# Kernel optimization log

Measured on AMD Instinct MI355X. Metric: run time of the kernel, lower is better.

The kernel has to match this reference:

```python
import jax, jax.numpy as jnp
import numpy as np

INIT_L = 512.0
EPS = 1e-6
N_HEAD = 16


def fire_bias(T, w1, b1, w2, b2, c, L_multiplier):
    # positions and relative distances
    pos = jnp.arange(T, dtype=jnp.float32)
    rel = pos[:, None] - pos[None, :]                      # (T, T)
    threshold = jnp.abs(L_multiplier * INIT_L)
    pos_norm = jnp.maximum(pos, threshold)[:, None]        # (T, 1)
    rel = jnp.log(jnp.abs(c * rel) + 1.0)                  # (T, T)
    pos_norm = jnp.log(jnp.abs(c * pos_norm) + 1.0) + EPS  # (T, 1)
    nd = rel / pos_norm                                    # (T, T)
    # tiny MLP: 1 -> mlp_width -> n_head
    h = jax.nn.relu(nd[..., None] * w1[0] + b1)            # (T, T, 32)
    bias = jnp.einsum('tsw,wh->hts', h, w2) + b2[:, None, None]  # (H, T, T)
    causal = jnp.tril(jnp.ones((T, T), dtype=bool))
    bias = jnp.where(causal[None], bias, -jnp.inf)
    return bias[None]                                      # (1, H, T, T)


def reference(x, Wqkv, bqkv, Wproj, bproj, w1, b1, w2, b2, c_param, L_multiplier):
    B, T, C = x.shape
    H = N_HEAD
    hd = C // H
    qkv = x @ Wqkv + bqkv                                  # (B, T, 3C)
    q, k, v = jnp.split(qkv, 3, axis=-1)
    q = q.reshape(B, T, H, hd).transpose(0, 2, 1, 3)       # (B, H, T, hd)
    k = k.reshape(B, T, H, hd).transpose(0, 2, 1, 3)
    v = v.reshape(B, T, H, hd).transpose(0, 2, 1, 3)
    bias = fire_bias(T, w1, b1, w2, b2, c_param, L_multiplier)  # (1, H, T, T)
    scale = 1.0 / jnp.sqrt(jnp.float32(hd))
    att = jnp.einsum('bhqd,bhkd->bhqk', q, k) * scale + bias
    att = jax.nn.softmax(att, axis=-1)
    y = jnp.einsum('bhqk,bhkd->bhqd', att, v)              # (B, H, T, hd)
    y = y.transpose(0, 2, 1, 3).reshape(B, T, C)
    return y @ Wproj + bproj


def setup_inputs() -> dict:
    key = jax.random.key(0)
    ks = jax.random.split(key, 8)
    B, T, C, H, W = 2, 2048, 1024, 16, 32
    s = 0.02
    return {
        'x': jax.random.normal(ks[0], (B, T, C), jnp.float32),
        'Wqkv': jax.random.normal(ks[1], (C, 3 * C), jnp.float32) * s,
        'bqkv': jnp.zeros((3 * C,), jnp.float32),
        'Wproj': jax.random.normal(ks[2], (C, C), jnp.float32) * s,
        'bproj': jnp.zeros((C,), jnp.float32),
        'w1': jax.random.normal(ks[3], (1, W), jnp.float32),
        'b1': jnp.zeros((W,), jnp.float32),
        'w2': jax.random.normal(ks[4], (W, H), jnp.float32) * 0.1,
        'b2': jnp.zeros((H,), jnp.float32),
        'c_param': jnp.float32(0.1),
        'L_multiplier': jnp.float32(1.0),
    }
```

## Files before the change

kernel.cpp:

```cpp
#include <hip/hip_runtime.h>
#include <cstdint>

typedef unsigned short u16;
typedef unsigned int u32;

typedef short bf16x8 __attribute__((ext_vector_type(8)));
typedef float f32x4 __attribute__((ext_vector_type(4)));

#define LN2 0.69314718055994530942f
#define LOG2E 1.44269504088896340736f
#define INFF __builtin_inff()

__device__ __forceinline__ u16 f2bf(float f) {
  u32 u = __float_as_uint(f);
  u = (u + 0x7fffu + ((u >> 16) & 1u)) >> 16;
  return (u16)u;
}
__device__ __forceinline__ u16 f2bfr(float f) {
  return (u16)((__float_as_uint(f) + 0x8000u) >> 16);
}
__device__ __forceinline__ u32 pack2bf(float a, float b) {
  u32 ta = __float_as_uint(a) + 0x8000u;
  u32 tb = __float_as_uint(b) + 0x8000u;
  return __builtin_amdgcn_perm(tb, ta, 0x07060302u);
}

#if __has_builtin(__builtin_amdgcn_global_load_lds)
#define HAVE_GLDS 1
__device__ __forceinline__ void glds16(const u16* g, u16* l) {
  __builtin_amdgcn_global_load_lds((const __attribute__((address_space(1))) void*)g,
                                   (__attribute__((address_space(3))) void*)l, 16, 0, 0);
}
#else
#define HAVE_GLDS 0
#endif


__global__ void k_convert_x(const float* __restrict__ in, u16* __restrict__ out, int n4) {
  int i = blockIdx.x * blockDim.x + threadIdx.x;
  if (i < n4) {
    float4 v = ((const float4*)in)[i];
    ushort4 o;
    o.x = f2bf(v.x); o.y = f2bf(v.y); o.z = f2bf(v.z); o.w = f2bf(v.w);
    ((ushort4*)out)[i] = o;
  }
}

__global__ void k_transpose_bf(const float* __restrict__ in, u16* __restrict__ out, int R, int C) {
  __shared__ float t[32][33];
  int c0 = blockIdx.x * 32, r0 = blockIdx.y * 32;
  int tx = threadIdx.x, ty = threadIdx.y;
#pragma unroll
  for (int k = 0; k < 4; k++) t[ty + 8 * k][tx] = in[(size_t)(r0 + ty + 8 * k) * C + c0 + tx];
  __syncthreads();
#pragma unroll
  for (int k = 0; k < 4; k++) out[(size_t)(c0 + ty + 8 * k) * R + r0 + tx] = f2bf(t[tx][ty + 8 * k]);
}

__global__ void k_tables(const float* __restrict__ cP, const float* __restrict__ lP,
                         float* __restrict__ ig2, float* __restrict__ rl) {
  int t = blockIdx.x * blockDim.x + threadIdx.x;
  float c = fabsf(cP[0]);
  if (t < 2048) {
    float lm = lP[0];
    float thr = fabsf(lm * 512.0f);
    float pn = fmaxf((float)t, thr);
    float den = logf(c * pn + 1.0f) + 1e-6f;
    ig2[t] = LN2 / den;
  }
  if (t < 2112) {
    int d = t - 63;
    if (d < 0) d = 0;
    rl[t] = log2f(c * (float)d + 1.0f);
  }
}

__global__ void k_segments(const float* __restrict__ w1, const float* __restrict__ b1,
                           const float* __restrict__ w2, const float* __restrict__ b2,
                           float* __restrict__ segX, float* __restrict__ segA,
                           float* __restrict__ segB, int* __restrict__ segU) {
  __shared__ float xs[32];
  __shared__ float srt[32];
  __shared__ float uniq[32];
  __shared__ int uCnt;
  int t = threadIdx.x;
  if (t < 32) {
    float w = w1[t], b = b1[t];
    xs[t] = (w != 0.0f) ? (-b / w) : INFF;
  }
  __syncthreads();
  if (t < 32) {
    float x = xs[t];
    int r = 0;
    for (int v = 0; v < 32; v++) {
      float xv = xs[v];
      if (xv < x || (xv == x && v < t)) r++;
    }
    srt[r] = x;
  }
  __syncthreads();
  if (t == 0) {
    int u = 0;
    for (int i = 0; i < 32; i++) {
      float v = srt[i];
      if (v < 3.0e38f && (u == 0 || v != uniq[u - 1])) uniq[u++] = v;
    }
    uCnt = u;
    segU[0] = u;
  }
  __syncthreads();
  int u = uCnt;
  if (t < u) segX[t] = uniq[t];
  for (int idx = t; idx < (u + 1) * 16; idx += blockDim.x) {
    int j = idx >> 4, h = idx & 15;
    float p;
    if (u == 0) p = 0.0f;
    else if (j == 0) p = uniq[0] - 1.0f;
    else if (j == u) p = uniq[u - 1] + 1.0f;
    else p = 0.5f * (uniq[j - 1] + uniq[j]);
    float A = b2[h], B = 0.0f;
    for (int w = 0; w < 32; w++) {
      float w1w = w1[w], b1w = b1[w], w2wh = w2[w * 16 + h];
      if (w1w != 0.0f) {
        if (fmaf(w1w, p, b1w) > 0.0f) { B += w1w * w2wh; A += b1w * w2wh; }
      } else if (b1w > 0.0f) {
        A += b1w * w2wh;
      }
    }
    segA[j * 16 + h] = A;
    segB[j * 16 + h] = B;
  }
}

template <int MODE>
__launch_bounds__(256, 3)
__global__ void k_gemm(const u16* __restrict__ A, const u16* __restrict__ BT,
                       const float* __restrict__ bias, float* __restrict__ outF,
                       u16* __restrict__ outQ, u16* __restrict__ outK, u16* __restrict__ outV,
                       int M, int N, int K) {
#if HAVE_GLDS
  __shared__ u16 As[128 * 64];
  __shared__ u16 Bs[128 * 64];
  const int tid = threadIdx.x;
  const int lane = tid & 63, wave = tid >> 6;
  const int li = lane & 15, quad = lane >> 4;
  const int wrow = (wave >> 1) * 64, wcol = (wave & 1) * 64;
  const int rb = blockIdx.y * 128, cb = blockIdx.x * 128;

  f32x4 acc[4][4];
#pragma unroll
  for (int i = 0; i < 4; i++)
#pragma unroll
    for (int j = 0; j < 4; j++) acc[i][j] = (f32x4){0.f, 0.f, 0.f, 0.f};

  const u16* gA = A + (size_t)(rb + (tid >> 3)) * K + (tid & 7) * 8;
  const u16* gB = BT + (size_t)(cb + (tid >> 3)) * K + (tid & 7) * 8;
  u16* lA = As + wave * 512;
  u16* lB = Bs + wave * 512;

  for (int k0 = 0; k0 < K; k0 += 64) {
    __syncthreads();
#pragma unroll
    for (int ch = 0; ch < 4; ch++) {
      glds16(gA + (size_t)ch * 32 * K + k0, lA + ch * 2048);
      glds16(gB + (size_t)ch * 32 * K + k0, lB + ch * 2048);
    }
    __syncthreads();
#pragma unroll
    for (int c = 0; c < 2; c++) {
      bf16x8 af[4], bfr[4];
#pragma unroll
      for (int mt = 0; mt < 4; mt++)
        af[mt] = *(const bf16x8*)(&As[(wrow + mt * 16 + li) * 64 + c * 32 + quad * 8]);
#pragma unroll
      for (int nt = 0; nt < 4; nt++)
        bfr[nt] = *(const bf16x8*)(&Bs[(wcol + nt * 16 + li) * 64 + c * 32 + quad * 8]);
#pragma unroll
      for (int mt = 0; mt < 4; mt++)
#pragma unroll
        for (int nt = 0; nt < 4; nt++)
          acc[mt][nt] = __builtin_amdgcn_mfma_f32_16x16x32_bf16(af[mt], bfr[nt], acc[mt][nt], 0, 0, 0);
    }
  }
#else
  __shared__ u16 As[128][72];
  __shared__ u16 Bs[128][72];
  const int tid = threadIdx.x;
  const int lane = tid & 63, wave = tid >> 6;
  const int li = lane & 15, quad = lane >> 4;
  const int wrow = (wave >> 1) * 64, wcol = (wave & 1) * 64;
  const int rb = blockIdx.y * 128, cb = blockIdx.x * 128;
  const int srow = tid >> 1, shalf = tid & 1;

  f32x4 acc[4][4];
#pragma unroll
  for (int i = 0; i < 4; i++)
#pragma unroll
    for (int j = 0; j < 4; j++) acc[i][j] = (f32x4){0.f, 0.f, 0.f, 0.f};

  const u16* gA = A + (size_t)(rb + srow) * K + shalf * 32;
  const u16* gB = BT + (size_t)(cb + srow) * K + shalf * 32;

  for (int k0 = 0; k0 < K; k0 += 64) {
    uint4 a0 = *(const uint4*)(gA + k0);
    uint4 a1 = *(const uint4*)(gA + k0 + 8);
    uint4 a2 = *(const uint4*)(gA + k0 + 16);
    uint4 a3 = *(const uint4*)(gA + k0 + 24);
    uint4 b0 = *(const uint4*)(gB + k0);
    uint4 b1 = *(const uint4*)(gB + k0 + 8);
    uint4 b2v = *(const uint4*)(gB + k0 + 16);
    uint4 b3 = *(const uint4*)(gB + k0 + 24);
    __syncthreads();
    *(uint4*)(&As[srow][shalf * 32]) = a0;
    *(uint4*)(&As[srow][shalf * 32 + 8]) = a1;
    *(uint4*)(&As[srow][shalf * 32 + 16]) = a2;
    *(uint4*)(&As[srow][shalf * 32 + 24]) = a3;
    *(uint4*)(&Bs[srow][shalf * 32]) = b0;
    *(uint4*)(&Bs[srow][shalf * 32 + 8]) = b1;
    *(uint4*)(&Bs[srow][shalf * 32 + 16]) = b2v;
    *(uint4*)(&Bs[srow][shalf * 32 + 24]) = b3;
    __syncthreads();
#pragma unroll
    for (int c = 0; c < 2; c++) {
      bf16x8 af[4], bfr[4];
#pragma unroll
      for (int mt = 0; mt < 4; mt++)
        af[mt] = *(const bf16x8*)(&As[wrow + mt * 16 + li][c * 32 + quad * 8]);
#pragma unroll
      for (int nt = 0; nt < 4; nt++)
        bfr[nt] = *(const bf16x8*)(&Bs[wcol + nt * 16 + li][c * 32 + quad * 8]);
#pragma unroll
      for (int mt = 0; mt < 4; mt++)
#pragma unroll
        for (int nt = 0; nt < 4; nt++)
          acc[mt][nt] = __builtin_amdgcn_mfma_f32_16x16x32_bf16(af[mt], bfr[nt], acc[mt][nt], 0, 0, 0);
    }
  }
#endif

#pragma unroll
  for (int mt = 0; mt < 4; mt++)
#pragma unroll
    for (int nt = 0; nt < 4; nt++)
#pragma unroll
      for (int r = 0; r < 4; r++) {
        int row = rb + wrow + mt * 16 + quad * 4 + r;
        int col = cb + wcol + nt * 16 + li;
        float v = acc[mt][nt][r] + bias[col];
        if (MODE == 0) {
          int b = row >> 11, tt = row & 2047;
          int sel = col >> 10, w = col & 1023, h = w >> 6, dd = w & 63;
          u16* dst = (sel == 0) ? outQ : ((sel == 1) ? outK : outV);
          dst[(size_t)((b * 16 + h) * 2048 + tt) * 64 + dd] = f2bf(v);
        } else {
          outF[(size_t)row * N + col] = v;
        }
      }
}

__launch_bounds__(256, 2)
__global__ void k_attn(const u16* __restrict__ Q, const u16* __restrict__ K,
                       const u16* __restrict__ V, u16* __restrict__ Y,
                       const float* __restrict__ ig2, const float* __restrict__ RL,
                       const float* __restrict__ segX, const float* __restrict__ segA,
                       const float* __restrict__ segB, const int* __restrict__ segU) {
  __shared__ u16 Ks[2][64][72];
  __shared__ u16 Vts[2][64][72];
  __shared__ u16 Ps[64][72];
  __shared__ float rls[2112];
  __shared__ float sXl[32];
  __shared__ float sAl[33];
  __shared__ float sBl[33];

  const int pr = blockIdx.x, h = blockIdx.y, b = blockIdx.z;
  const int tid = threadIdx.x, lane = tid & 63, wave = tid >> 6;
  const int li = lane & 15, quad = lane >> 4;
  const int bh = b * 16 + h;
  const u16* Qg = Q + (size_t)bh * 2048 * 64;
  const u16* Kg = K + (size_t)bh * 2048 * 64;
  const u16* Vg = V + (size_t)bh * 2048 * 64;

  for (int i = tid; i < 2112; i += 256) rls[i] = RL[i];

  const int u = segU[0];
  float x0 = INFF, A0, B0, A1, B1;
  A0 = segA[h]; B0 = segB[h]; A1 = A0; B1 = B0;
  if (u == 1) { x0 = segX[0]; A1 = segA[16 + h]; B1 = segB[16 + h]; }
  if (u > 1) {
    if (tid < u) sXl[tid] = segX[tid];
    if (tid < u + 1) { sAl[tid] = segA[tid * 16 + h]; sBl[tid] = segB[tid * 16 + h]; }
  }
  const float A0e = A0 * LOG2E, A1e = A1 * LOG2E;
  const float SCL = 0.125f * LOG2E;

  auto run_tile = [&](int qt) {
    const int qw = qt * 64 + wave * 16;
    const int t = qw + li;
    bf16x8 qf[2];
#pragma unroll
    for (int c = 0; c < 2; c++)
      qf[c] = *(const bf16x8*)(Qg + (size_t)t * 64 + c * 32 + quad * 8);

    const float gI = ig2[t];
    const float x0r = x0 / gI;
    const float B0g = B0 * gI * LOG2E, B1g = B1 * gI * LOG2E;
    float mrow = -INFF, lrow = 0.0f;
    f32x4 oacc[4];
#pragma unroll
    for (int nt = 0; nt < 4; nt++) oacc[nt] = (f32x4){0.f, 0.f, 0.f, 0.f};

    uint4 kv0, kv1, w0, w1;
    {
      const u16* ksrc = Kg + (size_t)(tid >> 2) * 64 + (tid & 3) * 16;
      kv0 = *(const uint4*)(ksrc);
      kv1 = *(const uint4*)(ksrc + 8);
      const u16* vsrc = Vg + (size_t)(2 * (tid & 31)) * 64 + (tid >> 5) * 8;
      w0 = *(const uint4*)(vsrc);
      w1 = *(const uint4*)(vsrc + 64);
    }
    __syncthreads();

    for (int kt = 0; kt <= qt; kt++) {
      const int kb = kt * 64, buf = kt & 1;
      *(uint4*)(&Ks[buf][tid >> 2][(tid & 3) * 16]) = kv0;
      *(uint4*)(&Ks[buf][tid >> 2][(tid & 3) * 16 + 8]) = kv1;
      {
        const int kkp = tid & 31, d0 = (tid >> 5) * 8;
        const u16* pw0 = (const u16*)&w0;
        const u16* pw1 = (const u16*)&w1;
#pragma unroll
        for (int j = 0; j < 8; j++)
          *(u32*)(&Vts[buf][d0 + j][2 * kkp]) = (u32)pw0[j] | ((u32)pw1[j] << 16);
      }
      __syncthreads();
      if (kt < qt) {
        const u16* ksrc = Kg + (size_t)(kb + 64 + (tid >> 2)) * 64 + (tid & 3) * 16;
        kv0 = *(const uint4*)(ksrc);
        kv1 = *(const uint4*)(ksrc + 8);
        const u16* vsrc = Vg + (size_t)(kb + 64 + 2 * (tid & 31)) * 64 + (tid >> 5) * 8;
        w0 = *(const uint4*)(vsrc);
        w1 = *(const uint4*)(vsrc + 64);
      }

      f32x4 sacc[4];
#pragma unroll
      for (int nt = 0; nt < 4; nt++) sacc[nt] = (f32x4){0.f, 0.f, 0.f, 0.f};
#pragma unroll
      for (int c = 0; c < 2; c++)
#pragma unroll
        for (int nt = 0; nt < 4; nt++) {
          bf16x8 kf = *(const bf16x8*)(&Ks[buf][nt * 16 + li][c * 32 + quad * 8]);
          sacc[nt] = __builtin_amdgcn_mfma_f32_16x16x32_bf16(kf, qf[c], sacc[nt], 0, 0, 0);
        }

      const int Cbase = t - kb - quad * 4 + 63;
      const float* rp = &rls[Cbase - 51];
      if (u <= 1) {
        const int lim = Cbase - 63;
#pragma unroll
        for (int nt = 0; nt < 4; nt++)
#pragma unroll
          for (int r = 0; r < 4; r++) {
            float rlv = rp[51 - nt * 16 - r];
            bool hi = rlv > x0r;
            float z = fmaf(rlv, hi ? B1g : B0g, hi ? A1e : A0e);
            z = fmaf(sacc[nt][r], SCL, z);
            if (kt == qt) z = (nt * 16 + r > lim) ? -INFF : z;
            sacc[nt][r] = z;
          }
      } else {
        const int lim = Cbase - 63;
#pragma unroll
        for (int nt = 0; nt < 4; nt++)
#pragma unroll
          for (int r = 0; r < 4; r++) {
            float nd = rp[51 - nt * 16 - r] * gI;
            int j = 0;
            for (int i = 0; i < u; i++) j += (nd > sXl[i]) ? 1 : 0;
            float z = (fmaf(nd, sBl[j], sAl[j]) + sacc[nt][r] * 0.125f) * LOG2E;
            if (kt == qt) z = (nt * 16 + r > lim) ? -INFF : z;
            sacc[nt][r] = z;
          }
      }

      float vm = -INFF;
#pragma unroll
      for (int nt = 0; nt < 4; nt++)
#pragma unroll
        for (int r = 0; r < 4; r++) vm = fmaxf(vm, sacc[nt][r]);
      vm = fmaxf(vm, __shfl_xor(vm, 16, 64));
      vm = fmaxf(vm, __shfl_xor(vm, 32, 64));
      float mnew = fmaxf(mrow, vm);
      float alpha = __builtin_amdgcn_exp2f(mrow - mnew);
      mrow = mnew;
      float s = 0.0f;
#pragma unroll
      for (int nt = 0; nt < 4; nt++)
#pragma unroll
        for (int r = 0; r < 4; r++) {
          float p = __builtin_amdgcn_exp2f(sacc[nt][r] - mnew);
          sacc[nt][r] = p;
          s += p;
        }
      s += __shfl_xor(s, 16, 64);
      s += __shfl_xor(s, 32, 64);
      lrow = lrow * alpha + s;
#pragma unroll
      for (int nt = 0; nt < 4; nt++)
#pragma unroll
        for (int r = 0; r < 4; r++) oacc[nt][r] *= alpha;

      const int prow = wave * 16 + li;
#pragma unroll
      for (int nt = 0; nt < 4; nt++) {
        uint2 pk;
        pk.x = pack2bf(sacc[nt][0], sacc[nt][1]);
        pk.y = pack2bf(sacc[nt][2], sacc[nt][3]);
        *(uint2*)(&Ps[prow][nt * 16 + quad * 4]) = pk;
      }

#pragma unroll
      for (int c = 0; c < 2; c++) {
        bf16x8 pf = *(const bf16x8*)(&Ps[wave * 16 + li][c * 32 + quad * 8]);
#pragma unroll
        for (int nt = 0; nt < 4; nt++) {
          bf16x8 vf = *(const bf16x8*)(&Vts[buf][nt * 16 + li][c * 32 + quad * 8]);
          oacc[nt] = __builtin_amdgcn_mfma_f32_16x16x32_bf16(vf, pf, oacc[nt], 0, 0, 0);
        }
      }
    }

    float inv = 1.0f / lrow;
    u16* dst = Y + (size_t)(b * 2048 + t) * 1024 + h * 64 + quad * 4;
#pragma unroll
    for (int nt = 0; nt < 4; nt++) {
      uint2 pk;
      pk.x = pack2bf(oacc[nt][0] * inv, oacc[nt][1] * inv);
      pk.y = pack2bf(oacc[nt][2] * inv, oacc[nt][3] * inv);
      *(uint2*)(dst + nt * 16) = pk;
    }
  };

  run_tile(pr);
  run_tile(31 - pr);
}

extern "C" void kernel_launch(void* const* d_in, const int* in_sizes, int n_in,
                              void* d_out, int out_size, void* d_ws, size_t ws_size,
                              hipStream_t stream) {
  (void)in_sizes; (void)n_in; (void)out_size; (void)ws_size;
  const float* x = (const float*)d_in[0];
  const float* Wqkv = (const float*)d_in[1];
  const float* bqkv = (const float*)d_in[2];
  const float* Wproj = (const float*)d_in[3];
  const float* bproj = (const float*)d_in[4];
  const float* w1 = (const float*)d_in[5];
  const float* b1 = (const float*)d_in[6];
  const float* w2 = (const float*)d_in[7];
  const float* b2 = (const float*)d_in[8];
  const float* cP = (const float*)d_in[9];
  const float* lP = (const float*)d_in[10];

  char* ws = (char*)d_ws;
  u16* Xbf = (u16*)(ws);
  u16* WqkvT = (u16*)(ws + (size_t)(8 << 20));
  u16* WprojT = (u16*)(ws + (size_t)(14 << 20));
  u16* Qb = (u16*)(ws + (size_t)(16 << 20));
  u16* Kb = (u16*)(ws + (size_t)(24 << 20));
  u16* Vb = (u16*)(ws + (size_t)(32 << 20));
  u16* Yb = (u16*)(ws + (size_t)(40 << 20));
  float* IG = (float*)(ws + (size_t)(48 << 20));
  float* RL = IG + 2048;
  float* SEGX = RL + 2112;
  float* SEGA = SEGX + 32;
  float* SEGB = SEGA + 33 * 16;
  int* SEGU = (int*)(SEGB + 33 * 16);

  k_convert_x<<<4096, 256, 0, stream>>>(x, Xbf, 1048576);
  k_transpose_bf<<<dim3(96, 32), dim3(32, 8), 0, stream>>>(Wqkv, WqkvT, 1024, 3072);
  k_transpose_bf<<<dim3(32, 32), dim3(32, 8), 0, stream>>>(Wproj, WprojT, 1024, 1024);
  k_tables<<<9, 256, 0, stream>>>(cP, lP, IG, RL);
  k_segments<<<1, 64, 0, stream>>>(w1, b1, w2, b2, SEGX, SEGA, SEGB, SEGU);

  k_gemm<0><<<dim3(24, 32), 256, 0, stream>>>(Xbf, WqkvT, bqkv, nullptr, Qb, Kb, Vb,
                                              4096, 3072, 1024);
  k_attn<<<dim3(16, 16, 2), 256, 0, stream>>>(Qb, Kb, Vb, Yb, IG, RL, SEGX, SEGA, SEGB, SEGU);
  k_gemm<1><<<dim3(8, 32), 256, 0, stream>>>(Yb, WprojT, bproj, (float*)d_out, nullptr, nullptr,
                                             nullptr, 4096, 1024, 1024);
}
```

Before: 243.5 us.

## Narrow output-projection GEMM tiles and single-buffer attention K/V for occupancy

The output-projection GEMM is templated on tile width and launched with 128x64 tiles, doubling its block count from 256 to 512 so the device is better filled. The attention kernel drops the double-buffered K/V shared tiles, which cuts LDS use, and raises its launch bound to 4 blocks per CU. It moves the barrier to the top of each key-tile iteration. The trade-off is an extra sync per key tile and less overlap between LDS writes and compute in attention. The narrower GEMM tile also gives less reuse of the A operand.

```diff
diff --git a/kernel.cpp b/kernel.cpp
--- a/kernel.cpp
+++ b/kernel.cpp
@@ -15,9 +15,6 @@
   u32 u = __float_as_uint(f);
   u = (u + 0x7fffu + ((u >> 16) & 1u)) >> 16;
   return (u16)u;
-}
-__device__ __forceinline__ u16 f2bfr(float f) {
-  return (u16)((__float_as_uint(f) + 0x8000u) >> 16);
 }
 __device__ __forceinline__ u32 pack2bf(float a, float b) {
   u32 ta = __float_as_uint(a) + 0x8000u;
@@ -132,27 +129,29 @@
   }
 }
 
-template <int MODE>
-__launch_bounds__(256, 3)
+template <int MODE, int BN>
+__launch_bounds__(256, (BN == 64) ? 4 : 3)
 __global__ void k_gemm(const u16* __restrict__ A, const u16* __restrict__ BT,
                        const float* __restrict__ bias, float* __restrict__ outF,
                        u16* __restrict__ outQ, u16* __restrict__ outK, u16* __restrict__ outV,
                        int M, int N, int K) {
-#if HAVE_GLDS
+  constexpr int NT = BN / 32;
+  constexpr int NCH = BN / 32;
   __shared__ u16 As[128 * 64];
-  __shared__ u16 Bs[128 * 64];
+  __shared__ u16 Bs[BN * 64];
   const int tid = threadIdx.x;
   const int lane = tid & 63, wave = tid >> 6;
   const int li = lane & 15, quad = lane >> 4;
-  const int wrow = (wave >> 1) * 64, wcol = (wave & 1) * 64;
-  const int rb = blockIdx.y * 128, cb = blockIdx.x * 128;
-
-  f32x4 acc[4][4];
+  const int wrow = (wave >> 1) * 64, wcol = (wave & 1) * (BN / 2);
+  const int rb = blockIdx.y * 128, cb = blockIdx.x * BN;
+
+  f32x4 acc[4][NT];
 #pragma unroll
   for (int i = 0; i < 4; i++)
 #pragma unroll
-    for (int j = 0; j < 4; j++) acc[i][j] = (f32x4){0.f, 0.f, 0.f, 0.f};
-
+    for (int j = 0; j < NT; j++) acc[i][j] = (f32x4){0.f, 0.f, 0.f, 0.f};
+
+#if HAVE_GLDS
   const u16* gA = A + (size_t)(rb + (tid >> 3)) * K + (tid & 7) * 8;
   const u16* gB = BT + (size_t)(cb + (tid >> 3)) * K + (tid & 7) * 8;
   u16* lA = As + wave * 512;
@@ -161,78 +160,51 @@
   for (int k0 = 0; k0 < K; k0 += 64) {
     __syncthreads();
 #pragma unroll
-    for (int ch = 0; ch < 4; ch++) {
-      glds16(gA + (size_t)ch * 32 * K + k0, lA + ch * 2048);
-      glds16(gB + (size_t)ch * 32 * K + k0, lB + ch * 2048);
-    }
+    for (int ch = 0; ch < 4; ch++) glds16(gA + (size_t)ch * 32 * K + k0, lA + ch * 2048);
+#pragma unroll
+    for (int ch = 0; ch < NCH; ch++) glds16(gB + (size_t)ch * 32 * K + k0, lB + ch * 2048);
     __syncthreads();
 #pragma unroll
     for (int c = 0; c < 2; c++) {
-      bf16x8 af[4], bfr[4];
+      bf16x8 af[4], bfr[NT];
 #pragma unroll
       for (int mt = 0; mt < 4; mt++)
         af[mt] = *(const bf16x8*)(&As[(wrow + mt * 16 + li) * 64 + c * 32 + quad * 8]);
 #pragma unroll
-      for (int nt = 0; nt < 4; nt++)
+      for (int nt = 0; nt < NT; nt++)
         bfr[nt] = *(const bf16x8*)(&Bs[(wcol + nt * 16 + li) * 64 + c * 32 + quad * 8]);
 #pragma unroll
       for (int mt = 0; mt < 4; mt++)
 #pragma unroll
-        for (int nt = 0; nt < 4; nt++)
+        for (int nt = 0; nt < NT; nt++)
           acc[mt][nt] = __builtin_amdgcn_mfma_f32_16x16x32_bf16(af[mt], bfr[nt], acc[mt][nt], 0, 0, 0);
     }
   }
 #else
-  __shared__ u16 As[128][72];
-  __shared__ u16 Bs[128][72];
-  const int tid = threadIdx.x;
-  const int lane = tid & 63, wave = tid >> 6;
-  const int li = lane & 15, quad = lane >> 4;
-  const int wrow = (wave >> 1) * 64, wcol = (wave & 1) * 64;
-  const int rb = blockIdx.y * 128, cb = blockIdx.x * 128;
-  const int srow = tid >> 1, shalf = tid & 1;
-
-  f32x4 acc[4][4];
-#pragma unroll
-  for (int i = 0; i < 4; i++)
-#pragma unroll
-    for (int j = 0; j < 4; j++) acc[i][j] = (f32x4){0.f, 0.f, 0.f, 0.f};
-
-  const u16* gA = A + (size_t)(rb + srow) * K + shalf * 32;
-  const u16* gB = BT + (size_t)(cb + srow) * K + shalf * 32;
-
   for (int k0 = 0; k0 < K; k0 += 64) {
-    uint4 a0 = *(const uint4*)(gA + k0);
-    uint4 a1 = *(const uint4*)(gA + k0 + 8);
-    uint4 a2 = *(const uint4*)(gA + k0 + 16);
-    uint4 a3 = *(const uint4*)(gA + k0 + 24);
-    uint4 b0 = *(const uint4*)(gB + k0);
-    uint4 b1 = *(const uint4*)(gB + k0 + 8);
-    uint4 b2v = *(const uint4*)(gB + k0 + 16);
-    uint4 b3 = *(const uint4*)(gB + k0 + 24);
     __syncthreads();
-    *(uint4*)(&As[srow][shalf * 32]) = a0;
-    *(uint4*)(&As[srow][shalf * 32 + 8]) = a1;
-    *(uint4*)(&As[srow][shalf * 32 + 16]) = a2;
-    *(uint4*)(&As[srow][shalf * 32 + 24]) = a3;
-    *(uint4*)(&Bs[srow][shalf * 32]) = b0;
-    *(uint4*)(&Bs[srow][shalf * 32 + 8]) = b1;
-    *(uint4*)(&Bs[srow][shalf * 32 + 16]) = b2v;
-    *(uint4*)(&Bs[srow][shalf * 32 + 24]) = b3;
+    for (int idx = tid * 8; idx < 128 * 64; idx += 256 * 8) {
+      int rr = idx >> 6, cc = idx & 63;
+      *(uint4*)(&As[idx]) = *(const uint4*)(A + (size_t)(rb + rr) * K + k0 + cc);
+    }
+    for (int idx = tid * 8; idx < BN * 64; idx += 256 * 8) {
+      int rr = idx >> 6, cc = idx & 63;
+      *(uint4*)(&Bs[idx]) = *(const uint4*)(BT + (size_t)(cb + rr) * K + k0 + cc);
+    }
     __syncthreads();
 #pragma unroll
     for (int c = 0; c < 2; c++) {
-      bf16x8 af[4], bfr[4];
+      bf16x8 af[4], bfr[NT];
 #pragma unroll
       for (int mt = 0; mt < 4; mt++)
-        af[mt] = *(const bf16x8*)(&As[wrow + mt * 16 + li][c * 32 + quad * 8]);
-#pragma unroll
-      for (int nt = 0; nt < 4; nt++)
-        bfr[nt] = *(const bf16x8*)(&Bs[wcol + nt * 16 + li][c * 32 + quad * 8]);
+        af[mt] = *(const bf16x8*)(&As[(wrow + mt * 16 + li) * 64 + c * 32 + quad * 8]);
+#pragma unroll
+      for (int nt = 0; nt < NT; nt++)
+        bfr[nt] = *(const bf16x8*)(&Bs[(wcol + nt * 16 + li) * 64 + c * 32 + quad * 8]);
 #pragma unroll
       for (int mt = 0; mt < 4; mt++)
 #pragma unroll
-        for (int nt = 0; nt < 4; nt++)
+        for (int nt = 0; nt < NT; nt++)
           acc[mt][nt] = __builtin_amdgcn_mfma_f32_16x16x32_bf16(af[mt], bfr[nt], acc[mt][nt], 0, 0, 0);
     }
   }
@@ -241,7 +213,7 @@
 #pragma unroll
   for (int mt = 0; mt < 4; mt++)
 #pragma unroll
-    for (int nt = 0; nt < 4; nt++)
+    for (int nt = 0; nt < NT; nt++)
 #pragma unroll
       for (int r = 0; r < 4; r++) {
         int row = rb + wrow + mt * 16 + quad * 4 + r;
@@ -258,14 +230,14 @@
       }
 }
 
-__launch_bounds__(256, 2)
+__launch_bounds__(256, 4)
 __global__ void k_attn(const u16* __restrict__ Q, const u16* __restrict__ K,
                        const u16* __restrict__ V, u16* __restrict__ Y,
                        const float* __restrict__ ig2, const float* __restrict__ RL,
                        const float* __restrict__ segX, const float* __restrict__ segA,
                        const float* __restrict__ segB, const int* __restrict__ segU) {
-  __shared__ u16 Ks[2][64][72];
-  __shared__ u16 Vts[2][64][72];
+  __shared__ u16 Ks[64][72];
+  __shared__ u16 Vts[64][72];
   __shared__ u16 Ps[64][72];
   __shared__ float rls[2112];
   __shared__ float sXl[32];
@@ -318,19 +290,19 @@
       w0 = *(const uint4*)(vsrc);
       w1 = *(const uint4*)(vsrc + 64);
     }
-    __syncthreads();
 
     for (int kt = 0; kt <= qt; kt++) {
-      const int kb = kt * 64, buf = kt & 1;
-      *(uint4*)(&Ks[buf][tid >> 2][(tid & 3) * 16]) = kv0;
-      *(uint4*)(&Ks[buf][tid >> 2][(tid & 3) * 16 + 8]) = kv1;
+      const int kb = kt * 64;
+      __syncthreads();
+      *(uint4*)(&Ks[tid >> 2][(tid & 3) * 16]) = kv0;
+      *(uint4*)(&Ks[tid >> 2][(tid & 3) * 16 + 8]) = kv1;
       {
         const int kkp = tid & 31, d0 = (tid >> 5) * 8;
         const u16* pw0 = (const u16*)&w0;
         const u16* pw1 = (const u16*)&w1;
 #pragma unroll
         for (int j = 0; j < 8; j++)
-          *(u32*)(&Vts[buf][d0 + j][2 * kkp]) = (u32)pw0[j] | ((u32)pw1[j] << 16);
+          *(u32*)(&Vts[d0 + j][2 * kkp]) = (u32)pw0[j] | ((u32)pw1[j] << 16);
       }
       __syncthreads();
       if (kt < qt) {
@@ -349,7 +321,7 @@
       for (int c = 0; c < 2; c++)
 #pragma unroll
         for (int nt = 0; nt < 4; nt++) {
-          bf16x8 kf = *(const bf16x8*)(&Ks[buf][nt * 16 + li][c * 32 + quad * 8]);
+          bf16x8 kf = *(const bf16x8*)(&Ks[nt * 16 + li][c * 32 + quad * 8]);
           sacc[nt] = __builtin_amdgcn_mfma_f32_16x16x32_bf16(kf, qf[c], sacc[nt], 0, 0, 0);
         }
 
@@ -424,7 +396,7 @@
         bf16x8 pf = *(const bf16x8*)(&Ps[wave * 16 + li][c * 32 + quad * 8]);
 #pragma unroll
         for (int nt = 0; nt < 4; nt++) {
-          bf16x8 vf = *(const bf16x8*)(&Vts[buf][nt * 16 + li][c * 32 + quad * 8]);
+          bf16x8 vf = *(const bf16x8*)(&Vts[nt * 16 + li][c * 32 + quad * 8]);
           oacc[nt] = __builtin_amdgcn_mfma_f32_16x16x32_bf16(vf, pf, oacc[nt], 0, 0, 0);
         }
       }
@@ -482,9 +454,9 @@
   k_tables<<<9, 256, 0, stream>>>(cP, lP, IG, RL);
   k_segments<<<1, 64, 0, stream>>>(w1, b1, w2, b2, SEGX, SEGA, SEGB, SEGU);
 
-  k_gemm<0><<<dim3(24, 32), 256, 0, stream>>>(Xbf, WqkvT, bqkv, nullptr, Qb, Kb, Vb,
-                                              4096, 3072, 1024);
+  k_gemm<0, 128><<<dim3(24, 32), 256, 0, stream>>>(Xbf, WqkvT, bqkv, nullptr, Qb, Kb, Vb,
+                                                   4096, 3072, 1024);
   k_attn<<<dim3(16, 16, 2), 256, 0, stream>>>(Qb, Kb, Vb, Yb, IG, RL, SEGX, SEGA, SEGB, SEGU);
-  k_gemm<1><<<dim3(8, 32), 256, 0, stream>>>(Yb, WprojT, bproj, (float*)d_out, nullptr, nullptr,
-                                             nullptr, 4096, 1024, 1024);
-}
+  k_gemm<1, 64><<<dim3(16, 32), 256, 0, stream>>>(Yb, WprojT, bproj, (float*)d_out, nullptr,
+                                                  nullptr, nullptr, 4096, 1024, 1024);
+}
```

Result: slower. 285.1 us (+17.1%).
